# Kernel tuning notes

Hardware: AMD Instinct MI355X
Metric: run time of the kernel (lower is better)

## Reference

```python
import jax, jax.numpy as jnp
import numpy as np

L = 5          # num_layer
EMB = 128      # emb_dim
IN_DIM = 9     # input_dim
EDGE_DIM = 10
N_NODES = 50000
N_EDGES = 600000
N_GRAPHS = 512
BN_EPS = 1e-5


def _bn(x, g, b):
    # training-mode batch norm over axis 0 (biased variance, as torch)
    m = x.mean(axis=0)
    v = x.var(axis=0)
    return (x - m) * jax.lax.rsqrt(v + BN_EPS) * g + b


def setup_inputs() -> dict:
    key = jax.random.key(0)
    ks = jax.random.split(key, 20)
    s = 0.05
    d = {
        'x': jax.random.normal(ks[0], (N_NODES, IN_DIM), jnp.float32),
        'edge_index': jax.random.randint(ks[1], (2, N_EDGES), 0, N_NODES, jnp.int32),
        'edge_attr': jax.random.normal(ks[2], (N_EDGES, EDGE_DIM), jnp.float32),
        'batch': jnp.sort(jax.random.randint(ks[3], (N_NODES,), 0, N_GRAPHS, jnp.int32)),
        'node_W': jax.random.normal(ks[4], (IN_DIM, EMB)) * s,
        'node_b': jnp.zeros((EMB,)),
        'vn_emb': jnp.zeros((1, EMB)),                 # torch init: constant 0
        'eps': jnp.zeros((L,)),                        # GIN eps init 0
        'edge_W': jax.random.normal(ks[5], (L, EDGE_DIM, EMB)) * s,
        'edge_b': jnp.zeros((L, EMB)),
        'conv_W1': jax.random.normal(ks[6], (L, EMB, 2 * EMB)) * s,
        'conv_b1': jnp.zeros((L, 2 * EMB)),
        'conv_bn_g': jnp.ones((L, 2 * EMB)),
        'conv_bn_b': jnp.zeros((L, 2 * EMB)),
        'conv_W2': jax.random.normal(ks[7], (L, 2 * EMB, EMB)) * s,
        'conv_b2': jnp.zeros((L, EMB)),
        'bn_g': jnp.ones((L, EMB)),
        'bn_b': jnp.zeros((L, EMB)),
        'vmlp_W1': jax.random.normal(ks[8], (L - 1, EMB, 2 * EMB)) * s,
        'vmlp_b1': jnp.zeros((L - 1, 2 * EMB)),
        'vmlp_bn1_g': jnp.ones((L - 1, 2 * EMB)),
        'vmlp_bn1_b': jnp.zeros((L - 1, 2 * EMB)),
        'vmlp_W2': jax.random.normal(ks[9], (L - 1, 2 * EMB, EMB)) * s,
        'vmlp_b2': jnp.zeros((L - 1, EMB)),
        'vmlp_bn2_g': jnp.ones((L - 1, EMB)),
        'vmlp_bn2_b': jnp.zeros((L - 1, EMB)),
    }
    return d


def reference(x, edge_index, edge_attr, batch,
              node_W, node_b, vn_emb, eps, edge_W, edge_b,
              conv_W1, conv_b1, conv_bn_g, conv_bn_b, conv_W2, conv_b2,
              bn_g, bn_b,
              vmlp_W1, vmlp_b1, vmlp_bn1_g, vmlp_bn1_b,
              vmlp_W2, vmlp_b2, vmlp_bn2_g, vmlp_bn2_b):
    n = x.shape[0]
    src, dst = edge_index[0], edge_index[1]
    vn = jnp.broadcast_to(vn_emb[0], (N_GRAPHS, EMB))  # virtual node per graph
    h = x @ node_W + node_b                            # node encoder
    for l in range(L):
        h_in = h + vn[batch]                           # broadcast virtual node
        # DrugGINConv
        e = edge_attr @ edge_W[l] + edge_b[l]          # edge encoder [E,EMB]
        msg = jax.nn.relu(h_in[src] + e)               # gather + message
        agg = jax.ops.segment_sum(msg, dst, num_segments=n)  # scatter-add
        t = (1.0 + eps[l]) * h_in + agg
        t = _bn(t @ conv_W1[l] + conv_b1[l], conv_bn_g[l], conv_bn_b[l])
        t = jax.nn.relu(t) @ conv_W2[l] + conv_b2[l]
        t = _bn(t, bn_g[l], bn_b[l])                   # outer batch norm
        h = t if l == L - 1 else jax.nn.relu(t)        # dropout identity (p=0)
        if l < L - 1:
            vtmp = jax.ops.segment_sum(h_in, batch, num_segments=N_GRAPHS) + vn
            u = _bn(vtmp @ vmlp_W1[l] + vmlp_b1[l], vmlp_bn1_g[l], vmlp_bn1_b[l])
            u = jax.nn.relu(u) @ vmlp_W2[l] + vmlp_b2[l]
            vn = jax.nn.relu(_bn(u, vmlp_bn2_g[l], vmlp_bn2_b[l]))
    return h
```

## Files before the change

kernel.cpp:

```cpp
#include <hip/hip_runtime.h>


#define EMB 128
#define NGR 512
#define NLAYER 5
static constexpr float BN_EPS = 1e-5f;

typedef __attribute__((ext_vector_type(8))) short short8v;
typedef __attribute__((ext_vector_type(4))) float f32x4;

__device__ __forceinline__ ushort f2bf(float f) {
  union { float f; unsigned u; } c; c.f = f;
  return (ushort)((c.u + 0x7FFFu + ((c.u >> 16) & 1u)) >> 16);
}
__device__ __forceinline__ float bf2f(ushort h) {
  union { unsigned u; float f; } c; c.u = ((unsigned)h) << 16;
  return c.f;
}

struct __attribute__((aligned(32))) EPack {
  int src;
  ushort ea[10];
  ushort pad[3];
};


__global__ void init_kernel(int* __restrict__ deg, int ndeg,
                            float* __restrict__ stats, int nstats,
                            float* __restrict__ vn, const float* __restrict__ vn_emb) {
  int idx = blockIdx.x * blockDim.x + threadIdx.x;
  if (idx < ndeg) deg[idx] = 0;
  if (idx < nstats) stats[idx] = 0.f;
  if (idx < NGR * EMB) vn[idx] = vn_emb[idx & (EMB - 1)];
}

__global__ void deg_kernel(const int* __restrict__ ei, int* __restrict__ deg, int E) {
  int e = blockIdx.x * blockDim.x + threadIdx.x;
  if (e < E) atomicAdd(&deg[ei[E + e]], 1);
}


__global__ void scan1_kernel(const int* __restrict__ deg, int* __restrict__ bsum, int n) {
  __shared__ int ws[4];
  int t = threadIdx.x;
  int base = blockIdx.x * 2048 + t * 8;
  int s = 0;
  #pragma unroll
  for (int i = 0; i < 8; ++i) {
    int idx = base + i;
    if (idx < n) s += deg[idx];
  }
  #pragma unroll
  for (int off = 32; off; off >>= 1) s += __shfl_down(s, off);
  if ((t & 63) == 0) ws[t >> 6] = s;
  __syncthreads();
  if (t == 0) bsum[blockIdx.x] = ws[0] + ws[1] + ws[2] + ws[3];
}

__global__ void scan2_kernel(const int* __restrict__ bsum, int* __restrict__ boff,
                             int* __restrict__ row_n, int nb) {
  int t = threadIdx.x;
  int mine = (t < nb) ? bsum[t] : 0;
  int v = mine;
  #pragma unroll
  for (int off = 1; off < 64; off <<= 1) {
    int u = __shfl_up(v, off);
    if (t >= off) v += u;
  }
  if (t < nb) boff[t] = v - mine;
  if (t == nb - 1) *row_n = v;
}

__global__ __launch_bounds__(256) void scan3_kernel(const int* __restrict__ deg,
                                                    const int* __restrict__ boff,
                                                    int* __restrict__ row_start,
                                                    int* __restrict__ cursor, int n) {
  __shared__ int lsum[256];
  int t = threadIdx.x;
  int base = blockIdx.x * 2048 + t * 8;
  int loc[8];
  int s = 0;
  #pragma unroll
  for (int i = 0; i < 8; ++i) {
    int idx = base + i;
    int d = (idx < n) ? deg[idx] : 0;
    loc[i] = s;
    s += d;
  }
  lsum[t] = s;
  __syncthreads();
  #pragma unroll
  for (int off = 1; off < 256; off <<= 1) {
    int v2 = (t >= off) ? lsum[t - off] : 0;
    __syncthreads();
    lsum[t] += v2;
    __syncthreads();
  }
  int toff = boff[blockIdx.x] + lsum[t] - s;
  #pragma unroll
  for (int i = 0; i < 8; ++i) {
    int idx = base + i;
    if (idx < n) {
      int rs = toff + loc[i];
      row_start[idx] = rs;
      cursor[idx] = rs;
    }
  }
}

__global__ void fill_kernel(const int* __restrict__ ei, int* __restrict__ cursor,
                            const float* __restrict__ eattr,
                            EPack* __restrict__ epk, int E) {
  int e = blockIdx.x * blockDim.x + threadIdx.x;
  if (e < E) {
    int d = ei[E + e];
    int pos = atomicAdd(&cursor[d], 1);
    EPack r;
    r.src = ei[e];
    const float* ea = eattr + (size_t)e * 10;
    #pragma unroll
    for (int k = 0; k < 10; ++k) r.ea[k] = f2bf(ea[k]);
    r.pad[0] = r.pad[1] = r.pad[2] = 0;
    epk[pos] = r;
  }
}

__global__ void bounds_kernel(const int* __restrict__ batch, int* __restrict__ gstart,
                              int n, int ng) {
  int g = blockIdx.x * blockDim.x + threadIdx.x;
  if (g > ng) return;
  int lo = 0, hi = n;
  while (lo < hi) {
    int mid = (lo + hi) >> 1;
    if (batch[mid] < g) lo = mid + 1; else hi = mid;
  }
  gstart[g] = lo;
}

__global__ void wtrans_kernel(const float* __restrict__ W, ushort* __restrict__ Wth,
                              ushort* __restrict__ Wtl, int K, int N, int total) {
  int idx = blockIdx.x * blockDim.x + threadIdx.x;
  if (idx >= total) return;
  int kk = idx % K;
  int t = idx / K;
  int nn = t % N;
  int l = t / N;
  float v = W[((size_t)l * K + kk) * N + nn];
  ushort h = f2bf(v);
  Wth[idx] = h;
  Wtl[idx] = f2bf(v - bf2f(h));
}

__global__ void encoder_kernel(const float* __restrict__ x, const float* __restrict__ W,
                               const float* __restrict__ b, float* __restrict__ h0, int n) {
  __shared__ float Ws[9][EMB];
  __shared__ float bs[EMB];
  int t = threadIdx.x;
  if (t < EMB) {
    #pragma unroll
    for (int k = 0; k < 9; ++k) Ws[k][t] = W[k * EMB + t];
    bs[t] = b[t];
  }
  __syncthreads();
  int total = n * EMB;
  for (int idx = blockIdx.x * blockDim.x + t; idx < total; idx += gridDim.x * blockDim.x) {
    int i = idx >> 7, j = idx & 127;
    const float* xr = x + i * 9;
    float acc = bs[j];
    #pragma unroll
    for (int k = 0; k < 9; ++k) acc = fmaf(xr[k], Ws[k][j], acc);
    h0[idx] = acc;
  }
}


template <bool RAW>
__global__ void hin_kernel(const float* __restrict__ src, const float* __restrict__ vn,
                           const int* __restrict__ batch, const float* __restrict__ s2raw,
                           const float* __restrict__ g2, const float* __restrict__ b2,
                           float* __restrict__ h_in, ushort* __restrict__ h16, int n) {
  __shared__ float sc[EMB], sh[EMB];
  if (!RAW) {
    int j = threadIdx.x;
    if (j < EMB) {
      float s = s2raw[j], q = s2raw[EMB + j];
      float mean = s / (float)n;
      float var = q / (float)n - mean * mean;
      float scl = g2[j] * rsqrtf(var + BN_EPS);
      sc[j] = scl;
      sh[j] = b2[j] - mean * scl;
    }
    __syncthreads();
  }
  int total = n * EMB;
  for (int idx = blockIdx.x * blockDim.x + threadIdx.x; idx < total; idx += gridDim.x * blockDim.x) {
    int i = idx >> 7, j = idx & 127;
    float v = src[idx];
    if (!RAW) v = fmaxf(fmaf(v, sc[j], sh[j]), 0.f);
    float hv = v + vn[batch[i] * EMB + j];
    h_in[idx] = hv;
    h16[idx] = f2bf(hv);
  }
}

__global__ void out_kernel(const float* __restrict__ t2, const float* __restrict__ s2raw,
                           const float* __restrict__ g2, const float* __restrict__ b2,
                           float* __restrict__ out, int n) {
  __shared__ float sc[EMB], sh[EMB];
  int j0 = threadIdx.x;
  if (j0 < EMB) {
    float s = s2raw[j0], q = s2raw[EMB + j0];
    float mean = s / (float)n;
    float var = q / (float)n - mean * mean;
    float scl = g2[j0] * rsqrtf(var + BN_EPS);
    sc[j0] = scl;
    sh[j0] = b2[j0] - mean * scl;
  }
  __syncthreads();
  int total = n * EMB;
  for (int idx = blockIdx.x * blockDim.x + threadIdx.x; idx < total; idx += gridDim.x * blockDim.x) {
    int j = idx & 127;
    out[idx] = fmaf(t2[idx], sc[j], sh[j]);
  }
}

__global__ void vnsum_kernel(const float* __restrict__ h_in, const int* __restrict__ gstart,
                             const float* __restrict__ vn, float* __restrict__ vnsum) {
  int g = blockIdx.x;
  int j = threadIdx.x;
  int s0 = gstart[g], s1 = gstart[g + 1];
  float acc = vn[g * EMB + j];
  for (int i = s0; i < s1; ++i) acc += h_in[i * EMB + j];
  vnsum[g * EMB + j] = acc;
}

__global__ __launch_bounds__(128) void agg_kernel(
    const float* __restrict__ h_in, const ushort* __restrict__ h16,
    const int* __restrict__ row_start, const EPack* __restrict__ epk,
    const float* __restrict__ eW, const float* __restrict__ eb,
    const float* __restrict__ eps_p, int l,
    ushort* __restrict__ tpre_h, ushort* __restrict__ tpre_l, int n) {
  __shared__ float W[10][EMB];
  __shared__ float bia[EMB];
  int j = threadIdx.x;
  #pragma unroll
  for (int k = 0; k < 10; ++k) W[k][j] = eW[k * EMB + j];
  bia[j] = eb[j];
  float epsv = 1.f + eps_p[l];
  __syncthreads();

  int i = blockIdx.x;
  int s0 = row_start[i], s1 = row_start[i + 1];
  float acc = epsv * h_in[(size_t)i * EMB + j];
  int p = s0;
  for (; p + 8 <= s1; p += 8) {
    int srcs[8];
    #pragma unroll
    for (int u = 0; u < 8; ++u) srcs[u] = epk[p + u].src;
    float hv[8];
    #pragma unroll
    for (int u = 0; u < 8; ++u) hv[u] = bf2f(h16[(size_t)srcs[u] * EMB + j]);
    #pragma unroll
    for (int u = 0; u < 8; ++u) {
      const EPack* ep = epk + p + u;
      float v = bia[j];
      #pragma unroll
      for (int k = 0; k < 10; ++k) v = fmaf(bf2f(ep->ea[k]), W[k][j], v);
      acc += fmaxf(v + hv[u], 0.f);
    }
  }
  for (; p + 4 <= s1; p += 4) {
    int srcs[4];
    #pragma unroll
    for (int u = 0; u < 4; ++u) srcs[u] = epk[p + u].src;
    float hv[4];
    #pragma unroll
    for (int u = 0; u < 4; ++u) hv[u] = bf2f(h16[(size_t)srcs[u] * EMB + j]);
    #pragma unroll
    for (int u = 0; u < 4; ++u) {
      const EPack* ep = epk + p + u;
      float v = bia[j];
      #pragma unroll
      for (int k = 0; k < 10; ++k) v = fmaf(bf2f(ep->ea[k]), W[k][j], v);
      acc += fmaxf(v + hv[u], 0.f);
    }
  }
  for (; p < s1; ++p) {
    const EPack* ep = epk + p;
    float hv0 = bf2f(h16[(size_t)ep->src * EMB + j]);
    float v = bia[j];
    #pragma unroll
    for (int k = 0; k < 10; ++k) v = fmaf(bf2f(ep->ea[k]), W[k][j], v);
    acc += fmaxf(v + hv0, 0.f);
  }
  ushort hh = f2bf(acc);
  tpre_h[(size_t)i * EMB + j] = hh;
  tpre_l[(size_t)i * EMB + j] = f2bf(acc - bf2f(hh));
}

template <int KT, int NT, bool BN_A, bool STATS, bool APRE>
__global__ __launch_bounds__(256) void gemm_mfma(
    const float* __restrict__ A, const ushort* __restrict__ Ath,
    const ushort* __restrict__ Atl,
    const ushort* __restrict__ Bth, const ushort* __restrict__ Btl,
    const float* __restrict__ bias,
    float* __restrict__ C, int M,
    const float* __restrict__ bnraw, const float* __restrict__ bng,
    const float* __restrict__ bnb, float* __restrict__ statraw) {
  constexpr int BM = 128, BN = 128, BK = 32;
  constexpr int LDK = BK + 8;
  constexpr int KSTEPS = KT / BK;
  __shared__ ushort Ah[BM][LDK], Al[BM][LDK];
  __shared__ ushort Bh[BN][LDK], Bl[BN][LDK];
  __shared__ float red[8][BN], redq[8][BN];
  constexpr int SCN = BN_A ? KT : 1;
  __shared__ float scS[SCN], shS[SCN];

  int tid = threadIdx.x;
  if (BN_A) {
    for (int k = tid; k < KT; k += 256) {
      float s = bnraw[k], q = bnraw[KT + k];
      float mean = s / (float)M;
      float var = q / (float)M - mean * mean;
      float scl = bng[k] * rsqrtf(var + BN_EPS);
      scS[k] = scl;
      shS[k] = bnb[k] - mean * scl;
    }
  }

  int wv = tid >> 6, lane = tid & 63;
  int wr = wv >> 1, wc = wv & 1;
  int lr = lane & 15, kg = lane >> 4;
  int bm0 = blockIdx.x * BM;
  int gc0 = blockIdx.y * BN;

  int sr = tid >> 1;
  int skq = (tid & 1) * 16;

  f32x4 acc[4][4];
  #pragma unroll
  for (int fm = 0; fm < 4; ++fm)
    #pragma unroll
    for (int fn = 0; fn < 4; ++fn) {
      float b = bias[gc0 + wc * 64 + fn * 16 + lr];
      acc[fm][fn][0] = b; acc[fm][fn][1] = b; acc[fm][fn][2] = b; acc[fm][fn][3] = b;
    }

  for (int kt = 0; kt < KSTEPS; ++kt) {
    __syncthreads();
    {
      int grow = bm0 + sr;
      if (APRE) {
        short8v z;
        #pragma unroll
        for (int q2 = 0; q2 < 8; ++q2) z[q2] = 0;
        if (grow < M) {
          const ushort* aph = Ath + (size_t)grow * KT + kt * BK + skq;
          const ushort* apl = Atl + (size_t)grow * KT + kt * BK + skq;
          *(short8v*)&Ah[sr][skq] = *(const short8v*)aph;
          *(short8v*)&Ah[sr][skq + 8] = *(const short8v*)(aph + 8);
          *(short8v*)&Al[sr][skq] = *(const short8v*)apl;
          *(short8v*)&Al[sr][skq + 8] = *(const short8v*)(apl + 8);
        } else {
          *(short8v*)&Ah[sr][skq] = z;
          *(short8v*)&Ah[sr][skq + 8] = z;
          *(short8v*)&Al[sr][skq] = z;
          *(short8v*)&Al[sr][skq + 8] = z;
        }
      } else {
        const float* ap = A + (size_t)grow * KT + kt * BK + skq;
        short8v ah0, al0, ah1, al1;
        #pragma unroll
        for (int u = 0; u < 4; ++u) {
          float4 v = (grow < M) ? *reinterpret_cast<const float4*>(ap + u * 4)
                                : make_float4(0.f, 0.f, 0.f, 0.f);
          if (BN_A) {
            int gk = kt * BK + skq + u * 4;
            v.x = fmaxf(fmaf(v.x, scS[gk + 0], shS[gk + 0]), 0.f);
            v.y = fmaxf(fmaf(v.y, scS[gk + 1], shS[gk + 1]), 0.f);
            v.z = fmaxf(fmaf(v.z, scS[gk + 2], shS[gk + 2]), 0.f);
            v.w = fmaxf(fmaf(v.w, scS[gk + 3], shS[gk + 3]), 0.f);
          }
          float vv0 = v.x, vv1 = v.y, vv2 = v.z, vv3 = v.w;
          ushort h0 = f2bf(vv0), h1 = f2bf(vv1), h2 = f2bf(vv2), h3 = f2bf(vv3);
          ushort w0 = f2bf(vv0 - bf2f(h0)), w1 = f2bf(vv1 - bf2f(h1));
          ushort w2 = f2bf(vv2 - bf2f(h2)), w3 = f2bf(vv3 - bf2f(h3));
          if (u < 2) {
            ah0[u * 4 + 0] = (short)h0; ah0[u * 4 + 1] = (short)h1;
            ah0[u * 4 + 2] = (short)h2; ah0[u * 4 + 3] = (short)h3;
            al0[u * 4 + 0] = (short)w0; al0[u * 4 + 1] = (short)w1;
            al0[u * 4 + 2] = (short)w2; al0[u * 4 + 3] = (short)w3;
          } else {
            ah1[(u - 2) * 4 + 0] = (short)h0; ah1[(u - 2) * 4 + 1] = (short)h1;
            ah1[(u - 2) * 4 + 2] = (short)h2; ah1[(u - 2) * 4 + 3] = (short)h3;
            al1[(u - 2) * 4 + 0] = (short)w0; al1[(u - 2) * 4 + 1] = (short)w1;
            al1[(u - 2) * 4 + 2] = (short)w2; al1[(u - 2) * 4 + 3] = (short)w3;
          }
        }
        *(short8v*)&Ah[sr][skq] = ah0;
        *(short8v*)&Ah[sr][skq + 8] = ah1;
        *(short8v*)&Al[sr][skq] = al0;
        *(short8v*)&Al[sr][skq + 8] = al1;
      }
    }
    {
      const ushort* bph = Bth + (size_t)(gc0 + sr) * KT + kt * BK + skq;
      const ushort* bpl = Btl + (size_t)(gc0 + sr) * KT + kt * BK + skq;
      *(short8v*)&Bh[sr][skq] = *(const short8v*)bph;
      *(short8v*)&Bh[sr][skq + 8] = *(const short8v*)(bph + 8);
      *(short8v*)&Bl[sr][skq] = *(const short8v*)bpl;
      *(short8v*)&Bl[sr][skq + 8] = *(const short8v*)(bpl + 8);
    }
    __syncthreads();
    short8v a_h[4], a_l[4], b_h[4], b_l[4];
    #pragma unroll
    for (int f = 0; f < 4; ++f) {
      a_h[f] = *(const short8v*)&Ah[wr * 64 + f * 16 + lr][kg * 8];
      a_l[f] = *(const short8v*)&Al[wr * 64 + f * 16 + lr][kg * 8];
      b_h[f] = *(const short8v*)&Bh[wc * 64 + f * 16 + lr][kg * 8];
      b_l[f] = *(const short8v*)&Bl[wc * 64 + f * 16 + lr][kg * 8];
    }
    #pragma unroll
    for (int fm = 0; fm < 4; ++fm)
      #pragma unroll
      for (int fn = 0; fn < 4; ++fn) {
        acc[fm][fn] = __builtin_amdgcn_mfma_f32_16x16x32_bf16(a_h[fm], b_h[fn], acc[fm][fn], 0, 0, 0);
        acc[fm][fn] = __builtin_amdgcn_mfma_f32_16x16x32_bf16(a_h[fm], b_l[fn], acc[fm][fn], 0, 0, 0);
        acc[fm][fn] = __builtin_amdgcn_mfma_f32_16x16x32_bf16(a_l[fm], b_h[fn], acc[fm][fn], 0, 0, 0);
      }
  }

  #pragma unroll
  for (int fm = 0; fm < 4; ++fm) {
    int rb = bm0 + wr * 64 + fm * 16 + kg * 4;
    #pragma unroll
    for (int i = 0; i < 4; ++i) {
      int grow = rb + i;
      if (grow < M) {
        float* cp = C + (size_t)grow * NT + gc0 + wc * 64 + lr;
        #pragma unroll
        for (int fn = 0; fn < 4; ++fn) cp[fn * 16] = acc[fm][fn][i];
      }
    }
  }

  if (STATS) {
    #pragma unroll
    for (int fn = 0; fn < 4; ++fn) {
      float s = 0.f, q = 0.f;
      #pragma unroll
      for (int fm = 0; fm < 4; ++fm) {
        int rb = bm0 + wr * 64 + fm * 16 + kg * 4;
        #pragma unroll
        for (int i = 0; i < 4; ++i) {
          if (rb + i < M) {
            float v = acc[fm][fn][i];
            s += v;
            q = fmaf(v, v, q);
          }
        }
      }
      red[wr * 4 + kg][wc * 64 + fn * 16 + lr] = s;
      redq[wr * 4 + kg][wc * 64 + fn * 16 + lr] = q;
    }
    __syncthreads();
    if (tid < BN) {
      float s = 0.f, q = 0.f;
      #pragma unroll
      for (int r2 = 0; r2 < 8; ++r2) {
        s += red[r2][tid];
        q += redq[r2][tid];
      }
      int gcol = gc0 + tid;
      atomicAdd(&statraw[gcol], s);
      atomicAdd(&statraw[NT + gcol], q);
    }
  }
}


__global__ void vmlp1_kernel(const float* __restrict__ vtmp, const float* __restrict__ W,
                             const float* __restrict__ b, float* __restrict__ u1,
                             float* __restrict__ vs1raw) {
  __shared__ float a[EMB];
  int g = blockIdx.x;
  int j = threadIdx.x;
  if (j < EMB) a[j] = vtmp[g * EMB + j];
  __syncthreads();
  float acc = b[j];
  #pragma unroll 8
  for (int k = 0; k < EMB; ++k) acc = fmaf(a[k], W[k * 256 + j], acc);
  u1[g * 256 + j] = acc;
  atomicAdd(&vs1raw[j], acc);
  atomicAdd(&vs1raw[256 + j], acc * acc);
}

__global__ void vmlp2_kernel(const float* __restrict__ u1, const float* __restrict__ vs1raw,
                             const float* __restrict__ g1, const float* __restrict__ b1,
                             const float* __restrict__ W, const float* __restrict__ b2,
                             float* __restrict__ u2, float* __restrict__ vs2raw) {
  __shared__ float a[256];
  __shared__ float sc[256], sh[256];
  int g = blockIdx.x;
  int j = threadIdx.x;
  for (int k = j; k < 256; k += EMB) {
    float s = vs1raw[k], q = vs1raw[256 + k];
    float mean = s / (float)NGR;
    float var = q / (float)NGR - mean * mean;
    float scl = g1[k] * rsqrtf(var + BN_EPS);
    sc[k] = scl;
    sh[k] = b1[k] - mean * scl;
  }
  __syncthreads();
  for (int k = j; k < 256; k += EMB)
    a[k] = fmaxf(fmaf(u1[g * 256 + k], sc[k], sh[k]), 0.f);
  __syncthreads();
  float acc = b2[j];
  #pragma unroll 8
  for (int k = 0; k < 256; ++k) acc = fmaf(a[k], W[k * EMB + j], acc);
  u2[g * EMB + j] = acc;
  atomicAdd(&vs2raw[j], acc);
  atomicAdd(&vs2raw[EMB + j], acc * acc);
}

__global__ void vnupd_kernel(const float* __restrict__ u2, const float* __restrict__ vs2raw,
                             const float* __restrict__ g2, const float* __restrict__ b2,
                             float* __restrict__ vn) {
  __shared__ float sc[EMB], sh[EMB];
  int g = blockIdx.x;
  int j = threadIdx.x;
  {
    float s = vs2raw[j], q = vs2raw[EMB + j];
    float mean = s / (float)NGR;
    float var = q / (float)NGR - mean * mean;
    float scl = g2[j] * rsqrtf(var + BN_EPS);
    sc[j] = scl;
    sh[j] = b2[j] - mean * scl;
  }
  __syncthreads();
  vn[g * EMB + j] = fmaxf(fmaf(u2[g * EMB + j], sc[j], sh[j]), 0.f);
}


extern "C" void kernel_launch(void* const* d_in, const int* in_sizes, int n_in,
                              void* d_out, int out_size, void* d_ws, size_t ws_size,
                              hipStream_t stream) {
  const float* x        = (const float*)d_in[0];
  const int*   ei       = (const int*)d_in[1];
  const float* eattr    = (const float*)d_in[2];
  const int*   batch    = (const int*)d_in[3];
  const float* node_W   = (const float*)d_in[4];
  const float* node_b   = (const float*)d_in[5];
  const float* vn_emb   = (const float*)d_in[6];
  const float* eps      = (const float*)d_in[7];
  const float* edge_W   = (const float*)d_in[8];
  const float* edge_b   = (const float*)d_in[9];
  const float* conv_W1  = (const float*)d_in[10];
  const float* conv_b1  = (const float*)d_in[11];
  const float* cbn_g    = (const float*)d_in[12];
  const float* cbn_b    = (const float*)d_in[13];
  const float* conv_W2  = (const float*)d_in[14];
  const float* conv_b2  = (const float*)d_in[15];
  const float* bn_g     = (const float*)d_in[16];
  const float* bn_b     = (const float*)d_in[17];
  const float* vW1      = (const float*)d_in[18];
  const float* vb1      = (const float*)d_in[19];
  const float* vbn1_g   = (const float*)d_in[20];
  const float* vbn1_b   = (const float*)d_in[21];
  const float* vW2      = (const float*)d_in[22];
  const float* vb2      = (const float*)d_in[23];
  const float* vbn2_g   = (const float*)d_in[24];
  const float* vbn2_b   = (const float*)d_in[25];

  const int n = in_sizes[0] / 9;
  const int E = in_sizes[1] / 2;
  const int nb = (n + 2047) / 2048;

  char* p = (char*)d_ws;
  auto carve = [&](size_t bytes) {
    char* r = p;
    p += (bytes + 255) & ~(size_t)255;
    return r;
  };
  float* h_in   = (float*)carve((size_t)n * EMB * 4);
  ushort* h16   = (ushort*)carve((size_t)n * EMB * 2);
  float* t1     = (float*)carve((size_t)n * 256 * 4);
  float* t2     = (float*)carve((size_t)n * EMB * 4);
  ushort* tpre_h = (ushort*)carve((size_t)n * EMB * 2);
  ushort* tpre_l = (ushort*)carve((size_t)n * EMB * 2);
  float* vn     = (float*)carve((size_t)NGR * EMB * 4);
  float* vnsum  = (float*)carve((size_t)NGR * EMB * 4);
  float* u1     = (float*)carve((size_t)NGR * 256 * 4);
  float* u2     = (float*)carve((size_t)NGR * EMB * 4);
  float* stats  = (float*)carve((size_t)NLAYER * 1536 * 4);
  int* deg      = (int*)carve((size_t)n * 4);
  int* rstart   = (int*)carve((size_t)(n + 1) * 4);
  int* cursor   = (int*)carve((size_t)n * 4);
  EPack* epk    = (EPack*)carve((size_t)E * sizeof(EPack));
  int* gstart   = (int*)carve((size_t)(NGR + 1) * 4);
  int* bsum     = (int*)carve((size_t)64 * 4);
  int* boff     = (int*)carve((size_t)64 * 4);
  ushort* wt1h  = (ushort*)carve((size_t)NLAYER * 256 * 128 * 2);
  ushort* wt1l  = (ushort*)carve((size_t)NLAYER * 256 * 128 * 2);
  ushort* wt2h  = (ushort*)carve((size_t)NLAYER * 128 * 256 * 2);
  ushort* wt2l  = (ushort*)carve((size_t)NLAYER * 128 * 256 * 2);
  float* h0     = t1;

  auto s1  = [&](int l) { return stats + (size_t)l * 1536; };
  auto s2  = [&](int l) { return stats + (size_t)l * 1536 + 512; };
  auto vs1 = [&](int l) { return stats + (size_t)l * 1536 + 768; };
  auto vs2 = [&](int l) { return stats + (size_t)l * 1536 + 1280; };

  init_kernel<<<(NGR * EMB + 255) / 256, 256, 0, stream>>>(deg, n, stats, NLAYER * 1536, vn, vn_emb);
  deg_kernel<<<(E + 255) / 256, 256, 0, stream>>>(ei, deg, E);
  scan1_kernel<<<nb, 256, 0, stream>>>(deg, bsum, n);
  scan2_kernel<<<1, 64, 0, stream>>>(bsum, boff, rstart + n, nb);
  scan3_kernel<<<nb, 256, 0, stream>>>(deg, boff, rstart, cursor, n);
  fill_kernel<<<(E + 255) / 256, 256, 0, stream>>>(ei, cursor, eattr, epk, E);
  bounds_kernel<<<(NGR + 1 + 255) / 256, 256, 0, stream>>>(batch, gstart, n, NGR);
  {
    int tot1 = NLAYER * 128 * 256;
    wtrans_kernel<<<(tot1 + 255) / 256, 256, 0, stream>>>(conv_W1, wt1h, wt1l, 128, 256, tot1);
    int tot2 = NLAYER * 256 * 128;
    wtrans_kernel<<<(tot2 + 255) / 256, 256, 0, stream>>>(conv_W2, wt2h, wt2l, 256, 128, tot2);
  }
  encoder_kernel<<<2048, 256, 0, stream>>>(x, node_W, node_b, h0, n);

  const int mtiles = (n + 127) / 128;

  for (int l = 0; l < NLAYER; ++l) {
    if (l == 0)
      hin_kernel<true><<<4096, 256, 0, stream>>>(h0, vn, batch, nullptr, nullptr, nullptr,
                                                 h_in, h16, n);
    else
      hin_kernel<false><<<4096, 256, 0, stream>>>(t2, vn, batch, s2(l - 1),
                                                  bn_g + (size_t)(l - 1) * EMB,
                                                  bn_b + (size_t)(l - 1) * EMB, h_in, h16, n);
    if (l < NLAYER - 1)
      vnsum_kernel<<<NGR, EMB, 0, stream>>>(h_in, gstart, vn, vnsum);

    agg_kernel<<<n, EMB, 0, stream>>>(h_in, h16, rstart, epk,
                                      edge_W + (size_t)l * 10 * EMB,
                                      edge_b + (size_t)l * EMB, eps, l, tpre_h, tpre_l, n);

    gemm_mfma<128, 256, false, true, true><<<dim3(mtiles, 2), 256, 0, stream>>>(
        nullptr, tpre_h, tpre_l, wt1h + (size_t)l * 256 * 128, wt1l + (size_t)l * 256 * 128,
        conv_b1 + (size_t)l * 256, t1, n, nullptr, nullptr, nullptr, s1(l));

    gemm_mfma<256, 128, true, true, false><<<dim3(mtiles, 1), 256, 0, stream>>>(
        t1, nullptr, nullptr, wt2h + (size_t)l * 128 * 256, wt2l + (size_t)l * 128 * 256,
        conv_b2 + (size_t)l * 128, t2, n,
        s1(l), cbn_g + (size_t)l * 256, cbn_b + (size_t)l * 256, s2(l));

    if (l < NLAYER - 1) {
      vmlp1_kernel<<<NGR, 256, 0, stream>>>(vnsum, vW1 + (size_t)l * 128 * 256,
                                            vb1 + (size_t)l * 256, u1, vs1(l));
      vmlp2_kernel<<<NGR, EMB, 0, stream>>>(u1, vs1(l), vbn1_g + (size_t)l * 256,
                                            vbn1_b + (size_t)l * 256,
                                            vW2 + (size_t)l * 256 * 128,
                                            vb2 + (size_t)l * EMB, u2, vs2(l));
      vnupd_kernel<<<NGR, EMB, 0, stream>>>(u2, vs2(l), vbn2_g + (size_t)l * EMB,
                                            vbn2_b + (size_t)l * EMB, vn);
    }
  }

  out_kernel<<<4096, 256, 0, stream>>>(t2, s2(NLAYER - 1),
                                       bn_g + (size_t)(NLAYER - 1) * EMB,
                                       bn_b + (size_t)(NLAYER - 1) * EMB,
                                       (float*)d_out, n);
}
```

Baseline: 1.271 ms.

## Use fp16 dot2 edge encoder, grid-stride aggregation, and split virtual-node sums

```diff
diff --git a/kernel.cpp b/kernel.cpp
--- a/kernel.cpp
+++ b/kernel.cpp
@@ -8,6 +8,13 @@
 
 typedef __attribute__((ext_vector_type(8))) short short8v;
 typedef __attribute__((ext_vector_type(4))) float f32x4;
+typedef _Float16 half2v __attribute__((ext_vector_type(2)));
+
+#if defined(__has_builtin)
+#if __has_builtin(__builtin_amdgcn_fdot2)
+#define HAS_FDOT2 1
+#endif
+#endif
 
 __device__ __forceinline__ ushort f2bf(float f) {
   union { float f; unsigned u; } c; c.f = f;
@@ -20,8 +27,8 @@
 
 struct __attribute__((aligned(32))) EPack {
   int src;
-  ushort ea[10];
-  ushort pad[3];
+  uint ea2[5];
+  uint pad[2];
 };
 
 
@@ -119,8 +126,13 @@
     r.src = ei[e];
     const float* ea = eattr + (size_t)e * 10;
     #pragma unroll
-    for (int k = 0; k < 10; ++k) r.ea[k] = f2bf(ea[k]);
-    r.pad[0] = r.pad[1] = r.pad[2] = 0;
+    for (int k2 = 0; k2 < 5; ++k2) {
+      union { uint u; half2v h; } cv;
+      cv.h[0] = (_Float16)ea[2 * k2];
+      cv.h[1] = (_Float16)ea[2 * k2 + 1];
+      r.ea2[k2] = cv.u;
+    }
+    r.pad[0] = r.pad[1] = 0;
     epk[pos] = r;
   }
 }
@@ -225,13 +237,17 @@
 }
 
 __global__ void vnsum_kernel(const float* __restrict__ h_in, const int* __restrict__ gstart,
-                             const float* __restrict__ vn, float* __restrict__ vnsum) {
+                             float* __restrict__ vnsum4) {
   int g = blockIdx.x;
+  int c = blockIdx.y;
   int j = threadIdx.x;
   int s0 = gstart[g], s1 = gstart[g + 1];
-  float acc = vn[g * EMB + j];
-  for (int i = s0; i < s1; ++i) acc += h_in[i * EMB + j];
-  vnsum[g * EMB + j] = acc;
+  int chunk = (s1 - s0 + 3) >> 2;
+  int a = s0 + c * chunk;
+  int b = min(s1, a + chunk);
+  float acc = 0.f;
+  for (int i = a; i < b; ++i) acc += h_in[(size_t)i * EMB + j];
+  vnsum4[((size_t)c * NGR + g) * EMB + j] = acc;
 }
 
 __global__ __launch_bounds__(128) void agg_kernel(
@@ -240,62 +256,72 @@
     const float* __restrict__ eW, const float* __restrict__ eb,
     const float* __restrict__ eps_p, int l,
     ushort* __restrict__ tpre_h, ushort* __restrict__ tpre_l, int n) {
-  __shared__ float W[10][EMB];
+  __shared__ uint Wp[5][EMB];
   __shared__ float bia[EMB];
   int j = threadIdx.x;
   #pragma unroll
-  for (int k = 0; k < 10; ++k) W[k][j] = eW[k * EMB + j];
+  for (int k2 = 0; k2 < 5; ++k2) {
+    union { uint u; half2v h; } cv;
+    cv.h[0] = (_Float16)eW[(2 * k2) * EMB + j];
+    cv.h[1] = (_Float16)eW[(2 * k2 + 1) * EMB + j];
+    Wp[k2][j] = cv.u;
+  }
   bia[j] = eb[j];
   float epsv = 1.f + eps_p[l];
   __syncthreads();
 
-  int i = blockIdx.x;
-  int s0 = row_start[i], s1 = row_start[i + 1];
-  float acc = epsv * h_in[(size_t)i * EMB + j];
-  int p = s0;
-  for (; p + 8 <= s1; p += 8) {
-    int srcs[8];
-    #pragma unroll
-    for (int u = 0; u < 8; ++u) srcs[u] = epk[p + u].src;
-    float hv[8];
-    #pragma unroll
-    for (int u = 0; u < 8; ++u) hv[u] = bf2f(h16[(size_t)srcs[u] * EMB + j]);
-    #pragma unroll
-    for (int u = 0; u < 8; ++u) {
-      const EPack* ep = epk + p + u;
+  for (int i = blockIdx.x; i < n; i += gridDim.x) {
+    int s0 = row_start[i], s1 = row_start[i + 1];
+    float acc = epsv * h_in[(size_t)i * EMB + j];
+    int p = s0;
+
+    auto edot = [&](const EPack* ep) -> float {
       float v = bia[j];
       #pragma unroll
-      for (int k = 0; k < 10; ++k) v = fmaf(bf2f(ep->ea[k]), W[k][j], v);
-      acc += fmaxf(v + hv[u], 0.f);
-    }
-  }
-  for (; p + 4 <= s1; p += 4) {
-    int srcs[4];
-    #pragma unroll
-    for (int u = 0; u < 4; ++u) srcs[u] = epk[p + u].src;
-    float hv[4];
-    #pragma unroll
-    for (int u = 0; u < 4; ++u) hv[u] = bf2f(h16[(size_t)srcs[u] * EMB + j]);
-    #pragma unroll
-    for (int u = 0; u < 4; ++u) {
-      const EPack* ep = epk + p + u;
-      float v = bia[j];
-      #pragma unroll
-      for (int k = 0; k < 10; ++k) v = fmaf(bf2f(ep->ea[k]), W[k][j], v);
-      acc += fmaxf(v + hv[u], 0.f);
-    }
-  }
-  for (; p < s1; ++p) {
-    const EPack* ep = epk + p;
-    float hv0 = bf2f(h16[(size_t)ep->src * EMB + j]);
-    float v = bia[j];
-    #pragma unroll
-    for (int k = 0; k < 10; ++k) v = fmaf(bf2f(ep->ea[k]), W[k][j], v);
-    acc += fmaxf(v + hv0, 0.f);
-  }
-  ushort hh = f2bf(acc);
-  tpre_h[(size_t)i * EMB + j] = hh;
-  tpre_l[(size_t)i * EMB + j] = f2bf(acc - bf2f(hh));
+      for (int k2 = 0; k2 < 5; ++k2) {
+        union { uint u; half2v h; } a, w;
+        a.u = ep->ea2[k2];
+        w.u = Wp[k2][j];
+#ifdef HAS_FDOT2
+        v = __builtin_amdgcn_fdot2(a.h, w.h, v, false);
+#else
+        v = fmaf((float)a.h[0], (float)w.h[0], v);
+        v = fmaf((float)a.h[1], (float)w.h[1], v);
+#endif
+      }
+      return v;
+    };
+
+    for (; p + 8 <= s1; p += 8) {
+      int srcs[8];
+      #pragma unroll
+      for (int u = 0; u < 8; ++u) srcs[u] = epk[p + u].src;
+      float hv[8];
+      #pragma unroll
+      for (int u = 0; u < 8; ++u) hv[u] = bf2f(h16[(size_t)srcs[u] * EMB + j]);
+      #pragma unroll
+      for (int u = 0; u < 8; ++u)
+        acc += fmaxf(edot(epk + p + u) + hv[u], 0.f);
+    }
+    for (; p + 4 <= s1; p += 4) {
+      int srcs[4];
+      #pragma unroll
+      for (int u = 0; u < 4; ++u) srcs[u] = epk[p + u].src;
+      float hv[4];
+      #pragma unroll
+      for (int u = 0; u < 4; ++u) hv[u] = bf2f(h16[(size_t)srcs[u] * EMB + j]);
+      #pragma unroll
+      for (int u = 0; u < 4; ++u)
+        acc += fmaxf(edot(epk + p + u) + hv[u], 0.f);
+    }
+    for (; p < s1; ++p) {
+      float hv0 = bf2f(h16[(size_t)epk[p].src * EMB + j]);
+      acc += fmaxf(edot(epk + p) + hv0, 0.f);
+    }
+    ushort hh = f2bf(acc);
+    tpre_h[(size_t)i * EMB + j] = hh;
+    tpre_l[(size_t)i * EMB + j] = f2bf(acc - bf2f(hh));
+  }
 }
 
 template <int KT, int NT, bool BN_A, bool STATS, bool APRE>
@@ -479,13 +505,19 @@
 }
 
 
-__global__ void vmlp1_kernel(const float* __restrict__ vtmp, const float* __restrict__ W,
+__global__ void vmlp1_kernel(const float* __restrict__ vnsum4, const float* __restrict__ vn,
+                             const float* __restrict__ W,
                              const float* __restrict__ b, float* __restrict__ u1,
                              float* __restrict__ vs1raw) {
   __shared__ float a[EMB];
   int g = blockIdx.x;
   int j = threadIdx.x;
-  if (j < EMB) a[j] = vtmp[g * EMB + j];
+  if (j < EMB) {
+    float s = vn[g * EMB + j];
+    #pragma unroll
+    for (int c = 0; c < 4; ++c) s += vnsum4[((size_t)c * NGR + g) * EMB + j];
+    a[j] = s;
+  }
   __syncthreads();
   float acc = b[j];
   #pragma unroll 8
@@ -589,7 +621,7 @@
   ushort* tpre_h = (ushort*)carve((size_t)n * EMB * 2);
   ushort* tpre_l = (ushort*)carve((size_t)n * EMB * 2);
   float* vn     = (float*)carve((size_t)NGR * EMB * 4);
-  float* vnsum  = (float*)carve((size_t)NGR * EMB * 4);
+  float* vnsum4 = (float*)carve((size_t)4 * NGR * EMB * 4);
   float* u1     = (float*)carve((size_t)NGR * 256 * 4);
   float* u2     = (float*)carve((size_t)NGR * EMB * 4);
   float* stats  = (float*)carve((size_t)NLAYER * 1536 * 4);
@@ -637,11 +669,11 @@
                                                   bn_g + (size_t)(l - 1) * EMB,
                                                   bn_b + (size_t)(l - 1) * EMB, h_in, h16, n);
     if (l < NLAYER - 1)
-      vnsum_kernel<<<NGR, EMB, 0, stream>>>(h_in, gstart, vn, vnsum);
-
-    agg_kernel<<<n, EMB, 0, stream>>>(h_in, h16, rstart, epk,
-                                      edge_W + (size_t)l * 10 * EMB,
-                                      edge_b + (size_t)l * EMB, eps, l, tpre_h, tpre_l, n);
+      vnsum_kernel<<<dim3(NGR, 4), EMB, 0, stream>>>(h_in, gstart, vnsum4);
+
+    agg_kernel<<<8192, EMB, 0, stream>>>(h_in, h16, rstart, epk,
+                                         edge_W + (size_t)l * 10 * EMB,
+                                         edge_b + (size_t)l * EMB, eps, l, tpre_h, tpre_l, n);
 
     gemm_mfma<128, 256, false, true, true><<<dim3(mtiles, 2), 256, 0, stream>>>(
         nullptr, tpre_h, tpre_l, wt1h + (size_t)l * 256 * 128, wt1l + (size_t)l * 256 * 128,
@@ -653,7 +685,7 @@
         s1(l), cbn_g + (size_t)l * 256, cbn_b + (size_t)l * 256, s2(l));
 
     if (l < NLAYER - 1) {
-      vmlp1_kernel<<<NGR, 256, 0, stream>>>(vnsum, vW1 + (size_t)l * 128 * 256,
+      vmlp1_kernel<<<NGR, 256, 0, stream>>>(vnsum4, vn, vW1 + (size_t)l * 128 * 256,
                                             vb1 + (size_t)l * 256, u1, vs1(l));
       vmlp2_kernel<<<NGR, EMB, 0, stream>>>(u1, vs1(l), vbn1_g + (size_t)l * 256,
                                             vbn1_b + (size_t)l * 256,
```

Result: faster. 1.131 ms (-11.0%).
